# Optimization experiments

Hardware: AMD Instinct MI355X
Metric: run time of the kernel (lower is better)

The kernel has to match this reference:

```python
import jax, jax.numpy as jnp
import numpy as np

N_NODES = 50000
N_EDGES = 800000
D_IN = 128
D_HID = 128
D_OUT = 64


def setup_inputs() -> dict:
    key = jax.random.key(0)
    ks = jax.random.split(key, 8)
    x = jax.random.normal(ks[0], (N_NODES, D_IN), dtype=jnp.float32)
    edge_index = jax.random.randint(ks[1], (2, N_EDGES), 0, N_NODES, dtype=jnp.int64)
    s = 1.0 / np.sqrt(D_HID)
    return {
        "x": x,
        "edge_index": edge_index,
        "W1": jax.random.normal(ks[2], (D_IN, D_HID), dtype=jnp.float32) * s,
        "b1": jnp.zeros((D_HID,), jnp.float32),
        "W2": jax.random.normal(ks[3], (D_HID, D_HID), dtype=jnp.float32) * s,
        "b2": jnp.zeros((D_HID,), jnp.float32),
        "W3": jax.random.normal(ks[4], (D_HID, D_HID), dtype=jnp.float32) * s,
        "b3": jnp.zeros((D_HID,), jnp.float32),
        "Wo1": jax.random.normal(ks[5], (D_HID, D_HID), dtype=jnp.float32) * s,
        "bo1": jnp.zeros((D_HID,), jnp.float32),
        "Wo2": jax.random.normal(ks[6], (D_HID, D_OUT), dtype=jnp.float32) * s,
        "bo2": jnp.zeros((D_OUT,), jnp.float32),
    }


def reference(x, edge_index, W1, b1, W2, b2, W3, b3, Wo1, bo1, Wo2, bo2):
    N = x.shape[0]
    src, dst = edge_index[0], edge_index[1]
    # GCN symmetric normalization with self-loops: deg_i = 1 + in_degree_i
    deg = jax.ops.segment_sum(jnp.ones(src.shape[0], x.dtype), dst, num_segments=N) + 1.0
    dis = jax.lax.rsqrt(deg)                      # deg^{-1/2}, [N]
    enorm = dis[src] * dis[dst]                   # per-edge norm, [E]
    self_norm = (dis * dis)[:, None]              # deg^{-1} for self-loops, [N,1]

    def gcn(h, W, b):
        h = h @ W                                 # [N, d_out]
        agg = jax.ops.segment_sum(h[src] * enorm[:, None], dst, num_segments=N)
        return agg + h * self_norm + b

    h = jax.nn.relu(gcn(x, W1, b1))
    h = jax.nn.relu(gcn(h, W2, b2))
    h = jax.nn.relu(gcn(h, W3, b3))
    # output MLP: two Linears, no activation between (as in the Sequential)
    return (h @ Wo1 + bo1) @ Wo2 + bo2
```

## Files before the change

kernel.cpp:

```cpp
#include <hip/hip_runtime.h>


#define DHID 128
#define NBUK 256
#define NBLK 196

typedef __attribute__((ext_vector_type(8))) short bf16x8;
typedef __attribute__((ext_vector_type(4))) float f32x4;

static __device__ __forceinline__ unsigned short f2bf(float f) {
  unsigned int u = __float_as_uint(f);
  u += 0x7fffu + ((u >> 16) & 1u);
  return (unsigned short)(u >> 16);
}
static __device__ __forceinline__ float bf_lo(unsigned int v) {
  return __uint_as_float(v << 16);
}
static __device__ __forceinline__ float bf_hi(unsigned int v) {
  return __uint_as_float(v & 0xffff0000u);
}

__global__ __launch_bounds__(256) void k_prep(const float* __restrict__ W1,
                                              const float* __restrict__ W2,
                                              const float* __restrict__ W3,
                                              const float* __restrict__ Wo1,
                                              const float* __restrict__ Wo2,
                                              unsigned short* __restrict__ W1t,
                                              unsigned short* __restrict__ W2t,
                                              unsigned short* __restrict__ W3t,
                                              unsigned short* __restrict__ Wo1t,
                                              unsigned short* __restrict__ Wo2t) {
  int b = blockIdx.x;
  int wi = b >> 3, part = b & 7;
  const float* src;
  unsigned short* dst;
  int N;
  switch (wi) {
    case 0: src = W1; dst = W1t; N = 128; break;
    case 1: src = W2; dst = W2t; N = 128; break;
    case 2: src = W3; dst = W3t; N = 128; break;
    case 3: src = Wo1; dst = Wo1t; N = 128; break;
    default: src = Wo2; dst = Wo2t; N = 64; break;
  }
  int cpp = N >> 3;
  int c0 = part * cpp;
  for (int idx = threadIdx.x; idx < cpp * 128; idx += 256) {
    int c = c0 + (idx >> 7);
    int k = idx & 127;
    dst[c * 128 + k] = f2bf(src[(size_t)k * N + c]);
  }
}

template <int NCOLS, int INF32, int OMODE>
__device__ __forceinline__ void mgemm_body(const void* __restrict__ Hsrc,
                                           const unsigned short* __restrict__ Wt,
                                           const float* __restrict__ bias,
                                           void* __restrict__ out, int M,
                                           int row0) {
  __shared__ unsigned short As[64][136];
  __shared__ unsigned short Ws[NCOLS][136];
  int tid = threadIdx.x;

  {
    int row = tid >> 2;
    int seg = tid & 3;
    int gr = row0 + row;
    if (INF32) {
      const float4* H4 = (const float4*)Hsrc;
#pragma unroll
      for (int i = 0; i < 8; i++) {
        float4 v = (gr < M) ? H4[(size_t)gr * 32 + seg * 8 + i]
                            : make_float4(0.f, 0.f, 0.f, 0.f);
        ushort4 o;
        o.x = f2bf(v.x); o.y = f2bf(v.y); o.z = f2bf(v.z); o.w = f2bf(v.w);
        *(ushort4*)&As[row][seg * 32 + i * 4] = o;
      }
    } else {
      const uint4* H4 = (const uint4*)Hsrc;
#pragma unroll
      for (int i = 0; i < 4; i++) {
        uint4 v = (gr < M) ? H4[(size_t)gr * 16 + seg * 4 + i]
                           : make_uint4(0u, 0u, 0u, 0u);
        *(uint4*)&As[row][seg * 32 + i * 8] = v;
      }
    }
  }
  {
    const uint4* Wt4 = (const uint4*)Wt;
    for (int idx = tid; idx < NCOLS * 16; idx += 256) {
      int c = idx >> 4, kk = idx & 15;
      *(uint4*)&Ws[c][kk * 8] = Wt4[idx];
    }
  }
  __syncthreads();

  int l = tid & 63;
  int w = tid >> 6;
  int mrow = l & 15;
  int kch = (l >> 4) * 8;

  f32x4 acc[NCOLS / 16];
#pragma unroll
  for (int c = 0; c < NCOLS / 16; c++) acc[c] = (f32x4){0.f, 0.f, 0.f, 0.f};

#pragma unroll
  for (int kk = 0; kk < 4; kk++) {
    bf16x8 a = *(const bf16x8*)&As[w * 16 + mrow][kk * 32 + kch];
#pragma unroll
    for (int c = 0; c < NCOLS / 16; c++) {
      bf16x8 b = *(const bf16x8*)&Ws[c * 16 + mrow][kk * 32 + kch];
      acc[c] = __builtin_amdgcn_mfma_f32_16x16x32_bf16(a, b, acc[c], 0, 0, 0);
    }
  }

  int rbase = row0 + w * 16 + (l >> 4) * 4;
#pragma unroll
  for (int c = 0; c < NCOLS / 16; c++) {
    int col = c * 16 + mrow;
    float bv = (OMODE != 0) ? bias[col] : 0.f;
#pragma unroll
    for (int r = 0; r < 4; r++) {
      int gr = rbase + r;
      if (gr < M) {
        float v = acc[c][r] + bv;
        if (OMODE == 2)
          ((float*)out)[(size_t)gr * NCOLS + col] = v;
        else
          ((unsigned short*)out)[(size_t)gr * 128 + col] = f2bf(v);
      }
    }
  }
}

template <int NCOLS, int INF32, int OMODE>
__global__ __launch_bounds__(256) void k_mgemm(const void* __restrict__ H,
                                               const unsigned short* __restrict__ Wt,
                                               const float* __restrict__ bias,
                                               void* __restrict__ out, int M) {
  mgemm_body<NCOLS, INF32, OMODE>(H, Wt, bias, out, M, (int)blockIdx.x * 64);
}

__global__ __launch_bounds__(256) void k_gemm1_hist(const float* __restrict__ x,
                                                    const unsigned short* __restrict__ W1t,
                                                    void* __restrict__ out, int M,
                                                    int nG, const int* __restrict__ ei,
                                                    int E, int EPB, int NPB,
                                                    int* __restrict__ Hist) {
  __shared__ int hs[NBUK];
  if ((int)blockIdx.x >= nG) {
    int tid = threadIdx.x;
    int j = (int)blockIdx.x - nG;
    hs[tid] = 0;
    __syncthreads();
    int e0 = j * EPB;
    int e1 = min(e0 + EPB, E);
    for (int e = e0 + tid; e < e1; e += 256) {
      int d = ei[E + e];
      atomicAdd(&hs[d / NPB], 1);
    }
    __syncthreads();
    Hist[tid * NBLK + j] = hs[tid];
    return;
  }
  mgemm_body<128, 1, 0>(x, W1t, nullptr, out, M, (int)blockIdx.x * 64);
}


__global__ __launch_bounds__(256) void k_scan1(const int* __restrict__ in,
                                               int* __restrict__ out,
                                               int* __restrict__ blk, int Mtot) {
  __shared__ int s[256];
  int tid = threadIdx.x;
  int i = blockIdx.x * 256 + tid;
  int v = (i < Mtot) ? in[i] : 0;
  s[tid] = v;
  __syncthreads();
  for (int off = 1; off < 256; off <<= 1) {
    int t = (tid >= off) ? s[tid - off] : 0;
    __syncthreads();
    s[tid] += t;
    __syncthreads();
  }
  if (i < Mtot) out[i] = s[tid] - v;
  if (tid == 255) blk[blockIdx.x] = s[255];
}

__global__ void k_scan2(int* blk, int n) {
  __shared__ int s[256];
  int tid = threadIdx.x;
  int v = (tid < n) ? blk[tid] : 0;
  s[tid] = v;
  __syncthreads();
  for (int off = 1; off < 256; off <<= 1) {
    int t = (tid >= off) ? s[tid - off] : 0;
    __syncthreads();
    s[tid] += t;
    __syncthreads();
  }
  if (tid < n) blk[tid] = s[tid] - v;
}

__global__ __launch_bounds__(256) void k_scatter(const int* __restrict__ ei, int E,
                                                 int EPB, int NPB,
                                                 const int* __restrict__ S,
                                                 const int* __restrict__ blk,
                                                 int2* __restrict__ sorted) {
  __shared__ int run[NBUK];
  int tid = threadIdx.x;
  int j = blockIdx.x;
  int idx = tid * NBLK + j;
  run[tid] = S[idx] + blk[idx >> 8];
  __syncthreads();
  int e0 = j * EPB;
  int e1 = min(e0 + EPB, E);
  for (int e = e0 + tid; e < e1; e += 256) {
    int s = ei[e];
    int d = ei[E + e];
    int slot = atomicAdd(&run[d / NPB], 1);
    sorted[slot] = make_int2(s, d);
  }
}

__global__ __launch_bounds__(256) void k_finalize(const int2* __restrict__ sorted,
                                                  const int* __restrict__ S,
                                                  const int* __restrict__ blk,
                                                  int E, int M, int NPB,
                                                  int* __restrict__ rp,
                                                  float* __restrict__ dis,
                                                  int* __restrict__ csr) {
  __shared__ int cnt[256];
  __shared__ int sc[256];
  int b = blockIdx.x;
  int tid = threadIdx.x;
  int node0 = b * NPB;
  int i0 = b * NBLK;
  int start = S[i0] + blk[i0 >> 8];
  int end;
  if (b == NBUK - 1) end = E;
  else {
    int i1 = i0 + NBLK;
    end = S[i1] + blk[i1 >> 8];
  }
  cnt[tid] = 0;
  __syncthreads();
  for (int i = start + tid; i < end; i += 256) {
    atomicAdd(&cnt[sorted[i].y - node0], 1);
  }
  __syncthreads();
  int v = cnt[tid];
  sc[tid] = v;
  __syncthreads();
  for (int off = 1; off < 256; off <<= 1) {
    int t = (tid >= off) ? sc[tid - off] : 0;
    __syncthreads();
    sc[tid] += t;
    __syncthreads();
  }
  int lrp = sc[tid] - v;
  int node = node0 + tid;
  if (tid < NPB && node < M) {
    rp[node] = start + lrp;
    dis[node] = rsqrtf((float)v + 1.0f);
  }
  if (b == NBUK - 1 && tid == 0) rp[M] = E;
  __syncthreads();
  cnt[tid] = lrp;
  __syncthreads();
  for (int i = start + tid; i < end; i += 256) {
    int2 p = sorted[i];
    int slot = atomicAdd(&cnt[p.y - node0], 1);
    csr[start + slot] = p.x;
  }
}

__global__ __launch_bounds__(256) void k_agg(const unsigned short* __restrict__ g,
                                             const int* __restrict__ csr,
                                             const int* __restrict__ rp,
                                             const float* __restrict__ dis,
                                             const float* __restrict__ bias,
                                             unsigned short* __restrict__ outh,
                                             int M) {
  int wid = (int)((blockIdx.x * 256 + threadIdx.x) >> 6);
  int lane = threadIdx.x & 63;
  if (wid >= M) return;
  const unsigned int* g1 = (const unsigned int*)g;
  float di = dis[wid];
  unsigned int self = g1[(size_t)wid * 64 + lane];
  float ax = di * bf_lo(self);
  float ay = di * bf_hi(self);
  int start = rp[wid], end = rp[wid + 1];
  for (int base = start; base < end; base += 64) {
    int n = end - base;
    if (n > 64) n = 64;
    int idx = 0;
    float dsv = 0.f;
    if (lane < n) {
      idx = csr[base + lane];
      dsv = dis[idx];
    }
    int jx = 0;
    for (; jx + 4 <= n; jx += 4) {
      int s0 = __shfl(idx, jx, 64);
      int s1 = __shfl(idx, jx + 1, 64);
      int s2 = __shfl(idx, jx + 2, 64);
      int s3 = __shfl(idx, jx + 3, 64);
      float d0 = __shfl(dsv, jx, 64);
      float d1 = __shfl(dsv, jx + 1, 64);
      float d2 = __shfl(dsv, jx + 2, 64);
      float d3 = __shfl(dsv, jx + 3, 64);
      unsigned int v0 = g1[(size_t)s0 * 64 + lane];
      unsigned int v1 = g1[(size_t)s1 * 64 + lane];
      unsigned int v2 = g1[(size_t)s2 * 64 + lane];
      unsigned int v3 = g1[(size_t)s3 * 64 + lane];
      ax = fmaf(d0, bf_lo(v0), ax);
      ay = fmaf(d0, bf_hi(v0), ay);
      ax = fmaf(d1, bf_lo(v1), ax);
      ay = fmaf(d1, bf_hi(v1), ay);
      ax = fmaf(d2, bf_lo(v2), ax);
      ay = fmaf(d2, bf_hi(v2), ay);
      ax = fmaf(d3, bf_lo(v3), ax);
      ay = fmaf(d3, bf_hi(v3), ay);
    }
    for (; jx < n; ++jx) {
      int s0 = __shfl(idx, jx, 64);
      float d0 = __shfl(dsv, jx, 64);
      unsigned int v = g1[(size_t)s0 * 64 + lane];
      ax = fmaf(d0, bf_lo(v), ax);
      ay = fmaf(d0, bf_hi(v), ay);
    }
  }
  float2 b = ((const float2*)bias)[lane];
  float rx = fmaxf(fmaf(di, ax, b.x), 0.f);
  float ry = fmaxf(fmaf(di, ay, b.y), 0.f);
  ushort2 o;
  o.x = f2bf(rx);
  o.y = f2bf(ry);
  ((ushort2*)outh)[(size_t)wid * 64 + lane] = o;
}


extern "C" void kernel_launch(void* const* d_in, const int* in_sizes, int n_in,
                              void* d_out, int out_size, void* d_ws, size_t ws_size,
                              hipStream_t stream) {
  const float* x = (const float*)d_in[0];
  const int* ei = (const int*)d_in[1];
  const float* W1 = (const float*)d_in[2];
  const float* b1 = (const float*)d_in[3];
  const float* W2 = (const float*)d_in[4];
  const float* b2 = (const float*)d_in[5];
  const float* W3 = (const float*)d_in[6];
  const float* b3 = (const float*)d_in[7];
  const float* Wo1 = (const float*)d_in[8];
  const float* bo1 = (const float*)d_in[9];
  const float* Wo2 = (const float*)d_in[10];
  const float* bo2 = (const float*)d_in[11];
  float* out = (float*)d_out;

  int M = in_sizes[0] / DHID;
  int E = in_sizes[1] / 2;

  int NPB = (M + NBUK - 1) / NBUK;
  int EPB = (E + NBLK - 1) / NBLK;
  int SCN = NBUK * NBLK;

  char* ws = (char*)d_ws;
  float* dis = (float*)(ws + 0);
  int* rp = (int*)(ws + (1ull << 20));
  int* Hist = (int*)(ws + (2ull << 20));
  int* S = (int*)(ws + (3ull << 20));
  int* blk = (int*)(ws + (4ull << 20));
  unsigned short* W1t = (unsigned short*)(ws + (4ull << 20) + 65536 + 0 * 32768);
  unsigned short* W2t = (unsigned short*)(ws + (4ull << 20) + 65536 + 1 * 32768);
  unsigned short* W3t = (unsigned short*)(ws + (4ull << 20) + 65536 + 2 * 32768);
  unsigned short* Wo1t = (unsigned short*)(ws + (4ull << 20) + 65536 + 3 * 32768);
  unsigned short* Wo2t = (unsigned short*)(ws + (4ull << 20) + 65536 + 4 * 32768);
  int* csr = (int*)(ws + (5ull << 20));
  unsigned short* gA = (unsigned short*)(ws + (9ull << 20));
  unsigned short* gB = (unsigned short*)(ws + (22ull << 20));
  unsigned short* hb = (unsigned short*)(ws + (35ull << 20));
  int2* sorted = (int2*)(ws + (48ull << 20));

  int gG = (M + 63) / 64;
  int gA4 = (M + 3) / 4;

  k_prep<<<40, 256, 0, stream>>>(W1, W2, W3, Wo1, Wo2, W1t, W2t, W3t, Wo1t, Wo2t);
  k_gemm1_hist<<<gG + NBLK, 256, 0, stream>>>(x, W1t, gA, M, gG, ei, E, EPB, NPB, Hist);
  k_scan1<<<NBLK, 256, 0, stream>>>(Hist, S, blk, SCN);
  k_scan2<<<1, 256, 0, stream>>>(blk, NBLK);
  k_scatter<<<NBLK, 256, 0, stream>>>(ei, E, EPB, NPB, S, blk, sorted);
  k_finalize<<<NBUK, 256, 0, stream>>>(sorted, S, blk, E, M, NPB, rp, dis, csr);

  k_agg<<<gA4, 256, 0, stream>>>(gA, csr, rp, dis, b1, hb, M);
  k_mgemm<128, 0, 0><<<gG, 256, 0, stream>>>(hb, W2t, nullptr, gB, M);
  k_agg<<<gA4, 256, 0, stream>>>(gB, csr, rp, dis, b2, hb, M);
  k_mgemm<128, 0, 0><<<gG, 256, 0, stream>>>(hb, W3t, nullptr, gA, M);
  k_agg<<<gA4, 256, 0, stream>>>(gA, csr, rp, dis, b3, hb, M);
  k_mgemm<128, 0, 1><<<gG, 256, 0, stream>>>(hb, Wo1t, bo1, gB, M);
  k_mgemm<64, 0, 2><<<gG, 256, 0, stream>>>(gB, Wo2t, bo2, out, M);
}
```

Measured before the change: 199.4 us.

## Vectorize GCN aggregation with 16-byte row loads and fold block scan into consumers

The aggregation kernel now splits each wavefront into four 16-lane groups. Each lane loads 16 bytes (8 bf16 values), so a wavefront fetches eight neighbor rows per iteration instead of one, and the partial sums are combined at the end with cross-lane shuffles. This aims to raise memory-level parallelism in the gather, which is bound by latency. Separately, the single-block k_scan2 launch is removed and every scatter and finalize block redoes the small block-offset scan in shared memory, trading repeated cheap work for one fewer launch and serialization point.

Result: slower. 207.5 us (+4.1%).

```diff
diff --git a/kernel.cpp b/kernel.cpp
--- a/kernel.cpp
+++ b/kernel.cpp
@@ -18,6 +18,16 @@
 }
 static __device__ __forceinline__ float bf_hi(unsigned int v) {
   return __uint_as_float(v & 0xffff0000u);
+}
+static __device__ __forceinline__ void fma8(float* acc, uint4 v, float s) {
+  acc[0] = fmaf(s, bf_lo(v.x), acc[0]);
+  acc[1] = fmaf(s, bf_hi(v.x), acc[1]);
+  acc[2] = fmaf(s, bf_lo(v.y), acc[2]);
+  acc[3] = fmaf(s, bf_hi(v.y), acc[3]);
+  acc[4] = fmaf(s, bf_lo(v.z), acc[4]);
+  acc[5] = fmaf(s, bf_hi(v.z), acc[5]);
+  acc[6] = fmaf(s, bf_lo(v.w), acc[6]);
+  acc[7] = fmaf(s, bf_hi(v.w), acc[7]);
 }
 
 __global__ __launch_bounds__(256) void k_prep(const float* __restrict__ W1,
@@ -185,19 +195,21 @@
   if (tid == 255) blk[blockIdx.x] = s[255];
 }
 
-__global__ void k_scan2(int* blk, int n) {
-  __shared__ int s[256];
-  int tid = threadIdx.x;
-  int v = (tid < n) ? blk[tid] : 0;
-  s[tid] = v;
+static __device__ __forceinline__ void scan_blk(const int* __restrict__ blk,
+                                                int* sblk, int tid) {
+  int bv = (tid < NBLK) ? blk[tid] : 0;
+  sblk[tid] = bv;
   __syncthreads();
   for (int off = 1; off < 256; off <<= 1) {
-    int t = (tid >= off) ? s[tid - off] : 0;
-    __syncthreads();
-    s[tid] += t;
-    __syncthreads();
-  }
-  if (tid < n) blk[tid] = s[tid] - v;
+    int t = (tid >= off) ? sblk[tid - off] : 0;
+    __syncthreads();
+    sblk[tid] += t;
+    __syncthreads();
+  }
+  int excl = sblk[tid] - bv;
+  __syncthreads();
+  sblk[tid] = excl;
+  __syncthreads();
 }
 
 __global__ __launch_bounds__(256) void k_scatter(const int* __restrict__ ei, int E,
@@ -206,10 +218,12 @@
                                                  const int* __restrict__ blk,
                                                  int2* __restrict__ sorted) {
   __shared__ int run[NBUK];
+  __shared__ int sblk[256];
   int tid = threadIdx.x;
   int j = blockIdx.x;
+  scan_blk(blk, sblk, tid);
   int idx = tid * NBLK + j;
-  run[tid] = S[idx] + blk[idx >> 8];
+  run[tid] = S[idx] + sblk[idx >> 8];
   __syncthreads();
   int e0 = j * EPB;
   int e1 = min(e0 + EPB, E);
@@ -230,16 +244,18 @@
                                                   int* __restrict__ csr) {
   __shared__ int cnt[256];
   __shared__ int sc[256];
+  __shared__ int sblk[256];
   int b = blockIdx.x;
   int tid = threadIdx.x;
+  scan_blk(blk, sblk, tid);
   int node0 = b * NPB;
   int i0 = b * NBLK;
-  int start = S[i0] + blk[i0 >> 8];
+  int start = S[i0] + sblk[i0 >> 8];
   int end;
   if (b == NBUK - 1) end = E;
   else {
     int i1 = i0 + NBLK;
-    end = S[i1] + blk[i1 >> 8];
+    end = S[i1] + sblk[i1 >> 8];
   }
   cnt[tid] = 0;
   __syncthreads();
@@ -283,59 +299,65 @@
   int wid = (int)((blockIdx.x * 256 + threadIdx.x) >> 6);
   int lane = threadIdx.x & 63;
   if (wid >= M) return;
-  const unsigned int* g1 = (const unsigned int*)g;
+  int grp = lane >> 4;
+  int sl = lane & 15;
+  const uint4* g4 = (const uint4*)g;
   float di = dis[wid];
-  unsigned int self = g1[(size_t)wid * 64 + lane];
-  float ax = di * bf_lo(self);
-  float ay = di * bf_hi(self);
+
+  float acc[8];
+#pragma unroll
+  for (int k = 0; k < 8; k++) acc[k] = 0.f;
+
+  {
+    uint4 v = g4[(size_t)wid * 16 + sl];
+    if (grp == 0) fma8(acc, v, di);
+  }
+
   int start = rp[wid], end = rp[wid + 1];
-  for (int base = start; base < end; base += 64) {
-    int n = end - base;
-    if (n > 64) n = 64;
-    int idx = 0;
-    float dsv = 0.f;
-    if (lane < n) {
-      idx = csr[base + lane];
-      dsv = dis[idx];
-    }
-    int jx = 0;
-    for (; jx + 4 <= n; jx += 4) {
-      int s0 = __shfl(idx, jx, 64);
-      int s1 = __shfl(idx, jx + 1, 64);
-      int s2 = __shfl(idx, jx + 2, 64);
-      int s3 = __shfl(idx, jx + 3, 64);
-      float d0 = __shfl(dsv, jx, 64);
-      float d1 = __shfl(dsv, jx + 1, 64);
-      float d2 = __shfl(dsv, jx + 2, 64);
-      float d3 = __shfl(dsv, jx + 3, 64);
-      unsigned int v0 = g1[(size_t)s0 * 64 + lane];
-      unsigned int v1 = g1[(size_t)s1 * 64 + lane];
-      unsigned int v2 = g1[(size_t)s2 * 64 + lane];
-      unsigned int v3 = g1[(size_t)s3 * 64 + lane];
-      ax = fmaf(d0, bf_lo(v0), ax);
-      ay = fmaf(d0, bf_hi(v0), ay);
-      ax = fmaf(d1, bf_lo(v1), ax);
-      ay = fmaf(d1, bf_hi(v1), ay);
-      ax = fmaf(d2, bf_lo(v2), ax);
-      ay = fmaf(d2, bf_hi(v2), ay);
-      ax = fmaf(d3, bf_lo(v3), ax);
-      ay = fmaf(d3, bf_hi(v3), ay);
-    }
-    for (; jx < n; ++jx) {
-      int s0 = __shfl(idx, jx, 64);
-      float d0 = __shfl(dsv, jx, 64);
-      unsigned int v = g1[(size_t)s0 * 64 + lane];
-      ax = fmaf(d0, bf_lo(v), ax);
-      ay = fmaf(d0, bf_hi(v), ay);
-    }
-  }
-  float2 b = ((const float2*)bias)[lane];
-  float rx = fmaxf(fmaf(di, ax, b.x), 0.f);
-  float ry = fmaxf(fmaf(di, ay, b.y), 0.f);
-  ushort2 o;
-  o.x = f2bf(rx);
-  o.y = f2bf(ry);
-  ((ushort2*)outh)[(size_t)wid * 64 + lane] = o;
+  for (int base = start; base < end; base += 8) {
+    int e0 = base + grp;
+    int e1 = e0 + 4;
+    int idx0 = wid, idx1 = wid;
+    float s0 = 0.f, s1 = 0.f;
+    if (e0 < end) {
+      idx0 = csr[e0];
+      s0 = dis[idx0];
+    }
+    if (e1 < end) {
+      idx1 = csr[e1];
+      s1 = dis[idx1];
+    }
+    uint4 v0 = g4[(size_t)idx0 * 16 + sl];
+    uint4 v1 = g4[(size_t)idx1 * 16 + sl];
+    fma8(acc, v0, s0);
+    fma8(acc, v1, s1);
+  }
+
+#pragma unroll
+  for (int k = 0; k < 8; k++) {
+    acc[k] += __shfl_xor(acc[k], 16, 64);
+    acc[k] += __shfl_xor(acc[k], 32, 64);
+  }
+
+  if (grp == 0) {
+    const float4* b4 = (const float4*)bias;
+    float4 ba = b4[sl * 2];
+    float4 bb = b4[sl * 2 + 1];
+    float r0 = fmaxf(fmaf(di, acc[0], ba.x), 0.f);
+    float r1 = fmaxf(fmaf(di, acc[1], ba.y), 0.f);
+    float r2 = fmaxf(fmaf(di, acc[2], ba.z), 0.f);
+    float r3 = fmaxf(fmaf(di, acc[3], ba.w), 0.f);
+    float r4 = fmaxf(fmaf(di, acc[4], bb.x), 0.f);
+    float r5 = fmaxf(fmaf(di, acc[5], bb.y), 0.f);
+    float r6 = fmaxf(fmaf(di, acc[6], bb.z), 0.f);
+    float r7 = fmaxf(fmaf(di, acc[7], bb.w), 0.f);
+    uint4 o;
+    o.x = (unsigned int)f2bf(r0) | ((unsigned int)f2bf(r1) << 16);
+    o.y = (unsigned int)f2bf(r2) | ((unsigned int)f2bf(r3) << 16);
+    o.z = (unsigned int)f2bf(r4) | ((unsigned int)f2bf(r5) << 16);
+    o.w = (unsigned int)f2bf(r6) | ((unsigned int)f2bf(r7) << 16);
+    ((uint4*)outh)[(size_t)wid * 16 + sl] = o;
+  }
 }
 
 
@@ -386,7 +408,6 @@
   k_prep<<<40, 256, 0, stream>>>(W1, W2, W3, Wo1, Wo2, W1t, W2t, W3t, Wo1t, Wo2t);
   k_gemm1_hist<<<gG + NBLK, 256, 0, stream>>>(x, W1t, gA, M, gG, ei, E, EPB, NPB, Hist);
   k_scan1<<<NBLK, 256, 0, stream>>>(Hist, S, blk, SCN);
-  k_scan2<<<1, 256, 0, stream>>>(blk, NBLK);
   k_scatter<<<NBLK, 256, 0, stream>>>(ei, E, EPB, NPB, S, blk, sorted);
   k_finalize<<<NBUK, 256, 0, stream>>>(sorted, S, blk, E, M, NPB, rp, dis, csr);
 
```

## Fold source-degree scaling into GEMM, fuse output MLP, inline block scan

Applied to the files above, without the earlier changes.

For layers two and three, the GEMM epilogue now multiplies each output row by its deg^{-1/2}. The following aggregation can then do plain sums without loading or shuffling per-neighbour dis values. The two output Linears are fused into one kernel that keeps the intermediate tile in shared memory, which removes one launch and an intermediate round-trip through global memory. The single-block scan2 launch is dropped by having scatter and finalize each rescan the block totals redundantly. The trade-off is extra bf16 rounding of the pre-scaled features and some duplicated scan work per block.

After: 202.3 us. No clear change (+1.4%).

```diff
diff --git a/kernel.cpp b/kernel.cpp
--- a/kernel.cpp
+++ b/kernel.cpp
@@ -55,6 +55,7 @@
 __device__ __forceinline__ void mgemm_body(const void* __restrict__ Hsrc,
                                            const unsigned short* __restrict__ Wt,
                                            const float* __restrict__ bias,
+                                           const float* __restrict__ dis,
                                            void* __restrict__ out, int M,
                                            int row0) {
   __shared__ unsigned short As[64][136];
@@ -117,12 +118,13 @@
 #pragma unroll
   for (int c = 0; c < NCOLS / 16; c++) {
     int col = c * 16 + mrow;
-    float bv = (OMODE != 0) ? bias[col] : 0.f;
+    float bv = (OMODE == 1 || OMODE == 2) ? bias[col] : 0.f;
 #pragma unroll
     for (int r = 0; r < 4; r++) {
       int gr = rbase + r;
       if (gr < M) {
         float v = acc[c][r] + bv;
+        if (OMODE == 3) v = acc[c][r] * dis[gr];
         if (OMODE == 2)
           ((float*)out)[(size_t)gr * NCOLS + col] = v;
         else
@@ -136,8 +138,102 @@
 __global__ __launch_bounds__(256) void k_mgemm(const void* __restrict__ H,
                                                const unsigned short* __restrict__ Wt,
                                                const float* __restrict__ bias,
+                                               const float* __restrict__ dis,
                                                void* __restrict__ out, int M) {
-  mgemm_body<NCOLS, INF32, OMODE>(H, Wt, bias, out, M, (int)blockIdx.x * 64);
+  mgemm_body<NCOLS, INF32, OMODE>(H, Wt, bias, dis, out, M, (int)blockIdx.x * 64);
+}
+
+__global__ __launch_bounds__(256) void k_mgemm2(const unsigned short* __restrict__ hb,
+                                                const unsigned short* __restrict__ Wo1t,
+                                                const float* __restrict__ bo1,
+                                                const unsigned short* __restrict__ Wo2t,
+                                                const float* __restrict__ bo2,
+                                                float* __restrict__ out, int M) {
+  __shared__ unsigned short As[64][136];
+  __shared__ unsigned short Ws[128][136];
+  int tid = threadIdx.x;
+  int row0 = (int)blockIdx.x * 64;
+
+  {
+    int row = tid >> 2, seg = tid & 3;
+    int gr = row0 + row;
+    const uint4* H4 = (const uint4*)hb;
+#pragma unroll
+    for (int i = 0; i < 4; i++) {
+      uint4 v = (gr < M) ? H4[(size_t)gr * 16 + seg * 4 + i]
+                         : make_uint4(0u, 0u, 0u, 0u);
+      *(uint4*)&As[row][seg * 32 + i * 8] = v;
+    }
+  }
+  {
+    const uint4* Wt4 = (const uint4*)Wo1t;
+    for (int idx = tid; idx < 128 * 16; idx += 256) {
+      int c = idx >> 4, kk = idx & 15;
+      *(uint4*)&Ws[c][kk * 8] = Wt4[idx];
+    }
+  }
+  __syncthreads();
+
+  int l = tid & 63;
+  int w = tid >> 6;
+  int mrow = l & 15;
+  int kch = (l >> 4) * 8;
+
+  f32x4 acc[8];
+#pragma unroll
+  for (int c = 0; c < 8; c++) acc[c] = (f32x4){0.f, 0.f, 0.f, 0.f};
+#pragma unroll
+  for (int kk = 0; kk < 4; kk++) {
+    bf16x8 a = *(const bf16x8*)&As[w * 16 + mrow][kk * 32 + kch];
+#pragma unroll
+    for (int c = 0; c < 8; c++) {
+      bf16x8 b = *(const bf16x8*)&Ws[c * 16 + mrow][kk * 32 + kch];
+      acc[c] = __builtin_amdgcn_mfma_f32_16x16x32_bf16(a, b, acc[c], 0, 0, 0);
+    }
+  }
+  __syncthreads();
+
+  {
+    int lrbase = w * 16 + (l >> 4) * 4;
+#pragma unroll
+    for (int c = 0; c < 8; c++) {
+      int col = c * 16 + mrow;
+      float bv = bo1[col];
+#pragma unroll
+      for (int r = 0; r < 4; r++)
+        As[lrbase + r][col] = f2bf(acc[c][r] + bv);
+    }
+    const uint4* Wt4 = (const uint4*)Wo2t;
+    for (int idx = tid; idx < 64 * 16; idx += 256) {
+      int c = idx >> 4, kk = idx & 15;
+      *(uint4*)&Ws[c][kk * 8] = Wt4[idx];
+    }
+  }
+  __syncthreads();
+
+  f32x4 a2[4];
+#pragma unroll
+  for (int c = 0; c < 4; c++) a2[c] = (f32x4){0.f, 0.f, 0.f, 0.f};
+#pragma unroll
+  for (int kk = 0; kk < 4; kk++) {
+    bf16x8 a = *(const bf16x8*)&As[w * 16 + mrow][kk * 32 + kch];
+#pragma unroll
+    for (int c = 0; c < 4; c++) {
+      bf16x8 b = *(const bf16x8*)&Ws[c * 16 + mrow][kk * 32 + kch];
+      a2[c] = __builtin_amdgcn_mfma_f32_16x16x32_bf16(a, b, a2[c], 0, 0, 0);
+    }
+  }
+  int rbase = row0 + w * 16 + (l >> 4) * 4;
+#pragma unroll
+  for (int c = 0; c < 4; c++) {
+    int col = c * 16 + mrow;
+    float bv = bo2[col];
+#pragma unroll
+    for (int r = 0; r < 4; r++) {
+      int gr = rbase + r;
+      if (gr < M) out[(size_t)gr * 64 + col] = a2[c][r] + bv;
+    }
+  }
 }
 
 __global__ __launch_bounds__(256) void k_gemm1_hist(const float* __restrict__ x,
@@ -162,7 +258,7 @@
     Hist[tid * NBLK + j] = hs[tid];
     return;
   }
-  mgemm_body<128, 1, 0>(x, W1t, nullptr, out, M, (int)blockIdx.x * 64);
+  mgemm_body<128, 1, 0>(x, W1t, nullptr, nullptr, out, M, (int)blockIdx.x * 64);
 }
 
 
@@ -185,19 +281,21 @@
   if (tid == 255) blk[blockIdx.x] = s[255];
 }
 
-__global__ void k_scan2(int* blk, int n) {
-  __shared__ int s[256];
-  int tid = threadIdx.x;
-  int v = (tid < n) ? blk[tid] : 0;
-  s[tid] = v;
+static __device__ __forceinline__ void scan_blk(const int* __restrict__ blk,
+                                                int* sblk, int tid) {
+  int bv = (tid < NBLK) ? blk[tid] : 0;
+  sblk[tid] = bv;
   __syncthreads();
   for (int off = 1; off < 256; off <<= 1) {
-    int t = (tid >= off) ? s[tid - off] : 0;
-    __syncthreads();
-    s[tid] += t;
-    __syncthreads();
-  }
-  if (tid < n) blk[tid] = s[tid] - v;
+    int t = (tid >= off) ? sblk[tid - off] : 0;
+    __syncthreads();
+    sblk[tid] += t;
+    __syncthreads();
+  }
+  int excl = sblk[tid] - bv;
+  __syncthreads();
+  sblk[tid] = excl;
+  __syncthreads();
 }
 
 __global__ __launch_bounds__(256) void k_scatter(const int* __restrict__ ei, int E,
@@ -206,10 +304,12 @@
                                                  const int* __restrict__ blk,
                                                  int2* __restrict__ sorted) {
   __shared__ int run[NBUK];
+  __shared__ int sblk[256];
   int tid = threadIdx.x;
   int j = blockIdx.x;
+  scan_blk(blk, sblk, tid);
   int idx = tid * NBLK + j;
-  run[tid] = S[idx] + blk[idx >> 8];
+  run[tid] = S[idx] + sblk[idx >> 8];
   __syncthreads();
   int e0 = j * EPB;
   int e1 = min(e0 + EPB, E);
@@ -230,16 +330,18 @@
                                                   int* __restrict__ csr) {
   __shared__ int cnt[256];
   __shared__ int sc[256];
+  __shared__ int sblk[256];
   int b = blockIdx.x;
   int tid = threadIdx.x;
+  scan_blk(blk, sblk, tid);
   int node0 = b * NPB;
   int i0 = b * NBLK;
-  int start = S[i0] + blk[i0 >> 8];
+  int start = S[i0] + sblk[i0 >> 8];
   int end;
   if (b == NBUK - 1) end = E;
   else {
     int i1 = i0 + NBLK;
-    end = S[i1] + blk[i1 >> 8];
+    end = S[i1] + sblk[i1 >> 8];
   }
   cnt[tid] = 0;
   __syncthreads();
@@ -273,6 +375,7 @@
   }
 }
 
+template <int GDIS>
 __global__ __launch_bounds__(256) void k_agg(const unsigned short* __restrict__ g,
                                              const int* __restrict__ csr,
                                              const int* __restrict__ rp,
@@ -286,8 +389,14 @@
   const unsigned int* g1 = (const unsigned int*)g;
   float di = dis[wid];
   unsigned int self = g1[(size_t)wid * 64 + lane];
-  float ax = di * bf_lo(self);
-  float ay = di * bf_hi(self);
+  float ax, ay;
+  if (GDIS) {
+    ax = di * bf_lo(self);
+    ay = di * bf_hi(self);
+  } else {
+    ax = bf_lo(self);
+    ay = bf_hi(self);
+  }
   int start = rp[wid], end = rp[wid + 1];
   for (int base = start; base < end; base += 64) {
     int n = end - base;
@@ -296,7 +405,7 @@
     float dsv = 0.f;
     if (lane < n) {
       idx = csr[base + lane];
-      dsv = dis[idx];
+      if (GDIS) dsv = dis[idx];
     }
     int jx = 0;
     for (; jx + 4 <= n; jx += 4) {
@@ -304,29 +413,39 @@
       int s1 = __shfl(idx, jx + 1, 64);
       int s2 = __shfl(idx, jx + 2, 64);
       int s3 = __shfl(idx, jx + 3, 64);
-      float d0 = __shfl(dsv, jx, 64);
-      float d1 = __shfl(dsv, jx + 1, 64);
-      float d2 = __shfl(dsv, jx + 2, 64);
-      float d3 = __shfl(dsv, jx + 3, 64);
       unsigned int v0 = g1[(size_t)s0 * 64 + lane];
       unsigned int v1 = g1[(size_t)s1 * 64 + lane];
       unsigned int v2 = g1[(size_t)s2 * 64 + lane];
       unsigned int v3 = g1[(size_t)s3 * 64 + lane];
-      ax = fmaf(d0, bf_lo(v0), ax);
-      ay = fmaf(d0, bf_hi(v0), ay);
-      ax = fmaf(d1, bf_lo(v1), ax);
-      ay = fmaf(d1, bf_hi(v1), ay);
-      ax = fmaf(d2, bf_lo(v2), ax);
-      ay = fmaf(d2, bf_hi(v2), ay);
-      ax = fmaf(d3, bf_lo(v3), ax);
-      ay = fmaf(d3, bf_hi(v3), ay);
+      if (GDIS) {
+        float d0 = __shfl(dsv, jx, 64);
+        float d1 = __shfl(dsv, jx + 1, 64);
+        float d2 = __shfl(dsv, jx + 2, 64);
+        float d3 = __shfl(dsv, jx + 3, 64);
+        ax = fmaf(d0, bf_lo(v0), ax);
+        ay = fmaf(d0, bf_hi(v0), ay);
+        ax = fmaf(d1, bf_lo(v1), ax);
+        ay = fmaf(d1, bf_hi(v1), ay);
+        ax = fmaf(d2, bf_lo(v2), ax);
+        ay = fmaf(d2, bf_hi(v2), ay);
+        ax = fmaf(d3, bf_lo(v3), ax);
+        ay = fmaf(d3, bf_hi(v3), ay);
+      } else {
+        ax += (bf_lo(v0) + bf_lo(v1)) + (bf_lo(v2) + bf_lo(v3));
+        ay += (bf_hi(v0) + bf_hi(v1)) + (bf_hi(v2) + bf_hi(v3));
+      }
     }
     for (; jx < n; ++jx) {
       int s0 = __shfl(idx, jx, 64);
-      float d0 = __shfl(dsv, jx, 64);
       unsigned int v = g1[(size_t)s0 * 64 + lane];
-      ax = fmaf(d0, bf_lo(v), ax);
-      ay = fmaf(d0, bf_hi(v), ay);
+      if (GDIS) {
+        float d0 = __shfl(dsv, jx, 64);
+        ax = fmaf(d0, bf_lo(v), ax);
+        ay = fmaf(d0, bf_hi(v), ay);
+      } else {
+        ax += bf_lo(v);
+        ay += bf_hi(v);
+      }
     }
   }
   float2 b = ((const float2*)bias)[lane];
@@ -386,15 +505,13 @@
   k_prep<<<40, 256, 0, stream>>>(W1, W2, W3, Wo1, Wo2, W1t, W2t, W3t, Wo1t, Wo2t);
   k_gemm1_hist<<<gG + NBLK, 256, 0, stream>>>(x, W1t, gA, M, gG, ei, E, EPB, NPB, Hist);
   k_scan1<<<NBLK, 256, 0, stream>>>(Hist, S, blk, SCN);
-  k_scan2<<<1, 256, 0, stream>>>(blk, NBLK);
   k_scatter<<<NBLK, 256, 0, stream>>>(ei, E, EPB, NPB, S, blk, sorted);
   k_finalize<<<NBUK, 256, 0, stream>>>(sorted, S, blk, E, M, NPB, rp, dis, csr);
 
-  k_agg<<<gA4, 256, 0, stream>>>(gA, csr, rp, dis, b1, hb, M);
-  k_mgemm<128, 0, 0><<<gG, 256, 0, stream>>>(hb, W2t, nullptr, gB, M);
-  k_agg<<<gA4, 256, 0, stream>>>(gB, csr, rp, dis, b2, hb, M);
-  k_mgemm<128, 0, 0><<<gG, 256, 0, stream>>>(hb, W3t, nullptr, gA, M);
-  k_agg<<<gA4, 256, 0, stream>>>(gA, csr, rp, dis, b3, hb, M);
-  k_mgemm<128, 0, 1><<<gG, 256, 0, stream>>>(hb, Wo1t, bo1, gB, M);
-  k_mgemm<64, 0, 2><<<gG, 256, 0, stream>>>(gB, Wo2t, bo2, out, M);
-}
+  k_agg<1><<<gA4, 256, 0, stream>>>(gA, csr, rp, dis, b1, hb, M);
+  k_mgemm<128, 0, 3><<<gG, 256, 0, stream>>>(hb, W2t, nullptr, dis, gB, M);
+  k_agg<0><<<gA4, 256, 0, stream>>>(gB, csr, rp, dis, b2, hb, M);
+  k_mgemm<128, 0, 3><<<gG, 256, 0, stream>>>(hb, W3t, nullptr, dis, gA, M);
+  k_agg<0><<<gA4, 256, 0, stream>>>(gA, csr, rp, dis, b3, hb, M);
+  k_mgemm2<<<gG, 256, 0, stream>>>(hb, Wo1t, bo1, Wo2t, bo2, out, M);
+}
```
